# Performance work log

Hardware: AMD Instinct MI355X
Metric: run time of the kernel (lower is better)

The kernel has to match this reference:

```python
import jax, jax.numpy as jnp
import numpy as np

B, N, C = 4, 32768, 64
D_IN = B * C          # 256 == in_channels * batch_size
D_MODEL = 256
HEADS = 2
NUM_EDGES = 4096
N_INC = 131072
EPS = 1e-5
NEG = 0.2


def _leaky(v):
    return jnp.where(v >= 0, v, NEG * v)


def _bn(v, g, b, m, var):  # BatchNorm1d, eval mode (running stats)
    return g * (v - m) * jax.lax.rsqrt(var + EPS) + b


def setup_inputs() -> dict:
    key = jax.random.key(0)
    ks = jax.random.split(key, 16)

    def lin_init(k, fan_in, shape):
        lim = 1.0 / np.sqrt(fan_in)
        return jax.random.uniform(k, shape, jnp.float32, -lim, lim)

    x = jax.random.normal(ks[0], (B, N, C), jnp.float32)
    row_n = jax.random.randint(ks[1], (N_INC,), 0, N, jnp.int32)
    row_e = jax.random.randint(ks[2], (N_INC,), 0, NUM_EDGES, jnp.int32)
    row_e = row_e.at[0].set(NUM_EDGES - 1)  # guarantee max edge id -> num_edges
    hyperedge_all = jnp.stack([row_n, row_e])

    return {
        "x": x,
        "hyperedge_all": hyperedge_all,
        # linear1: d_in -> d_model
        "W1": lin_init(ks[3], D_IN, (D_MODEL, D_IN)),
        "b1": lin_init(ks[4], D_IN, (D_MODEL,)),
        "bn1_g": 1.0 + 0.1 * jax.random.normal(ks[5], (D_MODEL,), jnp.float32),
        "bn1_b": 0.1 * jax.random.normal(ks[6], (D_MODEL,), jnp.float32),
        "bn1_m": 0.01 * jax.random.normal(ks[7], (D_MODEL,), jnp.float32),
        "bn1_v": jnp.ones((D_MODEL,), jnp.float32),
        # HypergraphConv lin: d_model -> heads*d_model (no bias); att: [heads, 2*d_model]
        "attW": lin_init(ks[8], D_MODEL, (HEADS * D_MODEL, D_MODEL)),
        "att": 0.1 * jax.random.normal(ks[9], (HEADS, 2 * D_MODEL), jnp.float32),
        "cb": 0.01 * jax.random.normal(ks[10], (D_MODEL,), jnp.float32),
        "bn2_g": 1.0 + 0.1 * jax.random.normal(ks[11], (D_MODEL,), jnp.float32),
        "bn2_b": 0.1 * jax.random.normal(ks[12], (D_MODEL,), jnp.float32),
        "bn2_m": 0.01 * jax.random.normal(ks[13], (D_MODEL,), jnp.float32),
        "bn2_v": jnp.ones((D_MODEL,), jnp.float32),
        # linear2: d_model -> d_in
        "W2": lin_init(ks[14], D_MODEL, (D_IN, D_MODEL)),
        "b2": lin_init(ks[15], D_MODEL, (D_IN,)),
        "ln_g": jnp.ones((C,), jnp.float32),
        "ln_b": jnp.zeros((C,), jnp.float32),
    }


def reference(x, hyperedge_all, W1, b1, bn1_g, bn1_b, bn1_m, bn1_v,
              attW, att, cb, bn2_g, bn2_b, bn2_m, bn2_v, W2, b2, ln_g, ln_b):
    src = x
    h = x.reshape(N, B * C)                               # [N, D_IN] (raw row-major reshape, as torch)
    h = _leaky(h @ W1.T + b1)                             # [N, D_MODEL]
    h = _bn(h, bn1_g, bn1_b, bn1_m, bn1_v)

    idx_n = hyperedge_all[0]                              # [I] node index per incidence
    idx_e = hyperedge_all[1]                              # [I] hyperedge index per incidence

    # hyperedge_attr = A^T h where A is the (0/1, duplicate-summed) incidence matrix
    eattr = jax.ops.segment_sum(h[idx_n], idx_e, NUM_EDGES)            # [E, D_MODEL]

    # --- HypergraphConv with attention, concat=False ---
    xh = (h @ attW.T).reshape(N, HEADS, D_MODEL)                       # [N, H, D]
    ea = (eattr @ attW.T).reshape(NUM_EDGES, HEADS, D_MODEL)           # [E, H, D]
    att_n, att_e = att[:, :D_MODEL], att[:, D_MODEL:]                  # [H, D] each
    sn = jnp.einsum('nhd,hd->nh', xh, att_n)                           # node score
    se = jnp.einsum('ehd,hd->eh', ea, att_e)                           # edge score
    alpha = _leaky(sn[idx_n] + se[idx_e])                              # [I, H]
    # segment softmax over destination nodes (PyG softmax(alpha, hyperedge_index[0]))
    amax = jax.ops.segment_max(alpha, idx_n, N)
    amax = jnp.where(jnp.isfinite(amax), amax, 0.0)
    ex = jnp.exp(alpha - amax[idx_n])
    denom = jax.ops.segment_sum(ex, idx_n, N)
    alpha = ex / (denom[idx_n] + 1e-16)                                # [I, H]

    ones_i = jnp.ones((N_INC,), h.dtype)
    deg_n = jax.ops.segment_sum(ones_i, idx_n, N)                      # D (hyperedge_weight = 1)
    Dinv = jnp.where(deg_n > 0, 1.0 / deg_n, 0.0)
    deg_e = jax.ops.segment_sum(ones_i, idx_e, NUM_EDGES)              # B
    Binv = jnp.where(deg_e > 0, 1.0 / deg_e, 0.0)

    # node -> edge: edge_out[e] = sum_inc B[e] * alpha * xh[n]
    m1 = Binv[idx_e][:, None, None] * alpha[:, :, None] * xh[idx_n]    # [I, H, D]
    edge_out = jax.ops.segment_sum(m1, idx_e, NUM_EDGES)               # [E, H, D]
    # edge -> node: node_out[n] = sum_inc D[n] * alpha * edge_out[e]
    m2 = Dinv[idx_n][:, None, None] * alpha[:, :, None] * edge_out[idx_e]
    node_out = jax.ops.segment_sum(m2, idx_n, N)                       # [N, H, D]
    x2 = node_out.mean(axis=1) + cb                                    # concat=False -> head mean + bias

    h = _bn(h + x2, bn2_g, bn2_b, bn2_m, bn2_v)
    h = _leaky(h @ W2.T + b2)                                          # [N, D_IN]

    y = src + h.reshape(B, N, C)                                       # residual (raw reshape back)
    mu = y.mean(-1, keepdims=True)                                     # LayerNorm over C
    var = jnp.mean((y - mu) ** 2, -1, keepdims=True)
    return ln_g * (y - mu) * jax.lax.rsqrt(var + EPS) + ln_b
```

## Files before the change

kernel.cpp:

```cpp
#include <hip/hip_runtime.h>

#define NN 32768
#define EE 4096
#define NI 131072
#define NEGS 0.2f
#define EPSV 1e-5f

typedef __bf16 bf16;
typedef __bf16 bf16x8 __attribute__((ext_vector_type(8)));
typedef __bf16 bf16x4 __attribute__((ext_vector_type(4)));
typedef float f32x4 __attribute__((ext_vector_type(4)));

#define AS1 __attribute__((address_space(1)))
#define AS3 __attribute__((address_space(3)))

__device__ __forceinline__ void gld16(const void* g, void* l) {
    __builtin_amdgcn_global_load_lds((const AS1 unsigned*)g, (AS3 unsigned*)l, 16, 0, 0);
}

__device__ __forceinline__ void stage_hl(const bf16* WH, const bf16* WL, bf16* sW,
                                         int buf, int kk, int wave, int lane) {
#pragma unroll
    for (int i = 0; i < 4; ++i) {
        size_t goff = (size_t)(wave*64 + lane)*256 + (size_t)kk*32 + i*8;
        size_t lb = (size_t)buf*16384 + (size_t)(i*256 + wave*64)*8;
        gld16(WH + goff, sW + lb);
        gld16(WL + goff, sW + 8192 + lb);
    }
}

__device__ __forceinline__ void stage_w(const bf16* WB, bf16* sW,
                                        int buf, int kk, int wave, int lane) {
#pragma unroll
    for (int i = 0; i < 4; ++i) {
        gld16(WB + (size_t)(wave*64 + lane)*256 + (size_t)kk*32 + i*8,
              sW + (size_t)buf*8192 + (size_t)(i*256 + wave*64)*8);
    }
}

constexpr size_t OFF_FLAGS = 0;
constexpr size_t OFF_W1F   = 32;
constexpr size_t OFF_WAF   = OFF_W1F + 65536;
constexpr size_t OFF_W2F   = OFF_WAF + 131072;
constexpr size_t OFF_SN    = OFF_W2F + 65536;
constexpr size_t OFF_SE    = OFF_SN + (size_t)NN*2;
constexpr size_t OFF_ALPHA = OFF_SE + (size_t)EE*2;
constexpr size_t OFF_DENOM = OFF_ALPHA + (size_t)NI*2;
constexpr size_t OFF_DEGN  = OFF_DENOM + (size_t)NN*2;
constexpr size_t OFF_DEGE  = OFF_DEGN + (size_t)NN;
constexpr size_t OFF_EATTR = OFF_DEGE + (size_t)EE;
constexpr size_t OFF_EOUT  = OFF_EATTR + (size_t)EE*256;
constexpr size_t OFF_H     = OFF_EOUT + (size_t)EE*512;
constexpr size_t OFF_WBA2  = OFF_H + (size_t)NN*256;
constexpr size_t OFF_WN    = OFF_WBA2 + 65536;
constexpr size_t OFF_WE    = OFF_WN + 512;
constexpr size_t OFF_ECOFF = OFF_WE + 512;
constexpr size_t OFF_ECURS = OFF_ECOFF + 4100;
constexpr size_t OFF_ECLIST= OFF_ECURS + (size_t)EE;
constexpr size_t WS_TOTAL  = OFF_ECLIST + (size_t)NI;

__device__ __forceinline__ float leaky(float v) { return v < 0.f ? NEGS * v : v; }

__device__ __forceinline__ float rdv(const void* p, size_t i, int f) {
    return f ? (float)((const bf16*)p)[i] : ((const float*)p)[i];
}

__device__ __forceinline__ void rd_idx(const void* p, int i, int mode, int& n, int& e) {
    if (mode == 0)      { n = ((const int*)p)[i];            e = ((const int*)p)[NI + i]; }
    else if (mode == 2) { n = ((const int*)p)[2*i];          e = ((const int*)p)[2*i + 1]; }
    else if (mode == 1) { n = (int)((const long long*)p)[i]; e = (int)((const long long*)p)[NI + i]; }
    else if (mode == 3) { n = (int)((const float*)p)[i];     e = (int)((const float*)p)[NI + i]; }
    else                { n = 0; e = 0; }
    if ((unsigned)n >= NN) n = 0;
    if ((unsigned)e >= EE) e = 0;
}

__global__ void detect_kernel(const void* p0, const void* p2, const void* p3, const void* p4,
                              const void* p5, const void* p6, const void* p7, const void* p8,
                              const void* p9, const void* p10, const void* p11, const void* p12,
                              const void* p13, const void* p14, const void* p15, const void* p16,
                              const void* p17, const void* p18, int* F) {
    __shared__ int cnt;
    int b = blockIdx.x, t = threadIdx.x;
    const void* ps[19] = {p0, nullptr, p2, p3, p4, p5, p6, p7, p8, p9, p10,
                          p11, p12, p13, p14, p15, p16, p17, p18};
    const int scan[19] = {2048, 0, 2048, 256, 256, 256, 256, 0, 2048, 1024,
                          256, 256, 256, 256, 0, 256, 256, 0, 0};
    if (b == 1)  { if (t == 0) { F[1] = 1; F[26] = 0; F[27] = 0; F[28] = 0; F[29] = 0; } return; }
    if (b == 18) { if (t == 0) F[18] = 1; return; }
    if (b == 7 || b == 14 || b == 17) {
        if (t == 0) F[b] = (*(const unsigned*)ps[b] == 0x3F803F80u) ? 1 : 0;
        return;
    }
    if (t == 0) cnt = 0;
    __syncthreads();
    int n = scan[b];
    int local = 0;
    for (int i = t; i < n; i += 256) {
        unsigned short u = ((const unsigned short*)ps[b])[i];
        if (((u >> 7) & 0xFFu) >= 0xC0u) local = 1;
    }
    if (local) atomicAdd(&cnt, 1);
    __syncthreads();
    if (t == 0) F[b] = (cnt == 0) ? 1 : 0;
}

__global__ void k_setflags(int* F) {
    if (threadIdx.x == 0) {
        F[25] = (!F[26]) ? 0 : (!F[28]) ? 2 : (!F[27]) ? 1 : (!F[29]) ? 3 : 99;
        int a = 1;
        const int ids[18] = {0,2,3,4,5,6,7,8,9,10,11,12,13,14,15,16,17,18};
        for (int k = 0; k < 18; ++k) a &= F[ids[k]];
        F[20] = a;
    }
}

__global__ void k_idxcheck(const void* p, int* F) {
    int i = blockIdx.x * 256 + threadIdx.x;
    const int*       p32 = (const int*)p;
    const long long* p64 = (const long long*)p;
    const float*     pf  = (const float*)p;
    int n0 = p32[i], e0 = p32[NI + i];
    if ((unsigned)n0 >= NN || (unsigned)e0 >= EE) atomicOr(&F[26], 1);
    int n2 = p32[2*i], e2 = p32[2*i + 1];
    if ((unsigned)n2 >= NN || (unsigned)e2 >= EE) atomicOr(&F[28], 1);
    long long n1 = p64[i], e1 = p64[NI + i];
    if (n1 < 0 || n1 >= NN || e1 < 0 || e1 >= EE) atomicOr(&F[27], 1);
    float nf = pf[i], ef = pf[NI + i];
    if (!(nf >= 0.f && nf < (float)NN && nf == floorf(nf)) ||
        !(ef >= 0.f && ef < (float)EE && ef == floorf(ef))) atomicOr(&F[29], 1);
}

__global__ void marker_kernel(float* OUT, int code) {
    size_t i = (size_t)blockIdx.x * 256 + threadIdx.x;
    OUT[i] = (i == 1) ? (float)code : 0.f;
}

__global__ void convb_kernel(const void* src, bf16* dst, const int* F, int fidx) {
    size_t i = ((size_t)blockIdx.x * 256 + threadIdx.x) * 4;
    if (F[fidx]) {
        *(bf16x4*)(dst + i) = *(const bf16x4*)((const bf16*)src + i);
    } else {
        f32x4 v = *(const f32x4*)((const float*)src + i);
        bf16x4 o;
        o[0] = (bf16)v[0]; o[1] = (bf16)v[1]; o[2] = (bf16)v[2]; o[3] = (bf16)v[3];
        *(bf16x4*)(dst + i) = o;
    }
}

__global__ void k_w1conv(const void* W1, const int* F, bf16* WH, bf16* WL) {
    size_t i = (size_t)blockIdx.x * 256 + threadIdx.x;
    float w = rdv(W1, i, F[2]);
    bf16 h = (bf16)w;
    WH[i] = h;
    WL[i] = (bf16)(w - (float)h);
}

__global__ void k_prep2(const void* g2, const void* be2, const void* m2, const void* v2,
                        const void* cb, const int* F, float* ST) {
    int k = threadIdx.x;
    float s = rdv(g2, k, F[11]) * rsqrtf(rdv(v2, k, F[14]) + EPSV);
    float t = s * (rdv(cb, k, F[10]) - rdv(m2, k, F[13])) + rdv(be2, k, F[12]);
    ST[k] = s; ST[256 + k] = t;
}

__global__ void k_w2conv(const void* W2, const void* b2, const float* ST, const int* F,
                         bf16* WH, bf16* WL, float* B2P) {
    __shared__ float sacc[4];
    int c = blockIdx.x, k = threadIdx.x;
    float w  = rdv(W2, (size_t)c*256 + k, F[15]);
    float sw = ST[k] * w;
    bf16 h = (bf16)sw;
    WH[(size_t)c*256 + k] = h;
    WL[(size_t)c*256 + k] = (bf16)(sw - (float)h);
    float p = ST[256 + k] * w;
#pragma unroll
    for (int m = 32; m >= 1; m >>= 1) p += __shfl_xor(p, m, 64);
    int lane = k & 63, wv = k >> 6;
    if (lane == 0) sacc[wv] = p;
    __syncthreads();
    if (k == 0) B2P[c] = rdv(b2, c, F[16]) + sacc[0] + sacc[1] + sacc[2] + sacc[3];
}

__global__ void k_fold(const void* attW, const void* att, const int* F,
                       float* WN, float* WE) {
    int c = threadIdx.x;
    int h = blockIdx.y;
    int d0 = blockIdx.x * 16;
    int faw = F[8], fat = F[9];
    float swn = 0.f, swe = 0.f;
#pragma unroll 4
    for (int dd = 0; dd < 16; ++dd) {
        int d = d0 + dd;
        float w = rdv(attW, (size_t)(h*256 + d)*256 + c, faw);
        swn += w * rdv(att, h*512 + d, fat);
        swe += w * rdv(att, h*512 + 256 + d, fat);
    }
    atomicAdd(&WN[h*256 + c], swn);
    atomicAdd(&WE[h*256 + c], swe);
}

__global__ void k_deg(const void* __restrict__ idx, float* __restrict__ DEGN,
                      float* __restrict__ DEGE, const int* __restrict__ F) {
    int i = blockIdx.x * 256 + threadIdx.x;
    int n, e; rd_idx(idx, i, F[25], n, e);
    atomicAdd(&DEGN[n], 1.f);
    atomicAdd(&DEGE[e], 1.f);
}

__global__ void scan_a(const float* __restrict__ DEGN, const float* __restrict__ DEGE,
                       int* __restrict__ BS) {
    __shared__ int wsum[4];
    int b = blockIdx.x, t = threadIdx.x, lane = t & 63, wave = t >> 6;
    const float* DEG = (b < 32) ? DEGN + (size_t)b*1024 : DEGE + (size_t)(b-32)*1024;
    f32x4 v = *(const f32x4*)(DEG + (size_t)t*4);
    int s = (int)v[0] + (int)v[1] + (int)v[2] + (int)v[3];
#pragma unroll
    for (int m = 32; m >= 1; m >>= 1) s += __shfl_xor(s, m, 64);
    if (lane == 0) wsum[wave] = s;
    __syncthreads();
    if (t == 0) BS[b] = wsum[0] + wsum[1] + wsum[2] + wsum[3];
}

__global__ void scan_b2(int* BS) {
    if (threadIdx.x == 0) { int run = 0; for (int i = 0;  i < 32; ++i) { int s = BS[i]; BS[i] = run; run += s; } }
    if (threadIdx.x == 1) { int run = 0; for (int i = 32; i < 36; ++i) { int s = BS[i]; BS[i] = run; run += s; } }
}

__global__ void scan_c(float* __restrict__ DEGN, float* __restrict__ DEGE,
                       const int* __restrict__ BS,
                       int* __restrict__ NOFF, int* __restrict__ NCURS,
                       int* __restrict__ ECOFF, int* __restrict__ ECURS) {
    __shared__ int wsum[4];
    int b = blockIdx.x, t = threadIdx.x, lane = t & 63, wave = t >> 6;
    bool isN = (b < 32);
    int bb = isN ? b : b - 32;
    float* DEG = isN ? DEGN + (size_t)bb*1024 : DEGE + (size_t)bb*1024;
    int* OFF   = isN ? NOFF + bb*1024 : ECOFF + bb*1024;
    int* CURS  = isN ? NCURS + bb*1024 : ECURS + bb*1024;
    f32x4 v = *(const f32x4*)(DEG + (size_t)t*4);
    int c0 = (int)v[0], c1 = (int)v[1], c2 = (int)v[2], c3 = (int)v[3];
    int s = c0 + c1 + c2 + c3;
    int p = s;
#pragma unroll
    for (int off = 1; off < 64; off <<= 1) {
        int u = __shfl_up(p, off, 64);
        if (lane >= off) p += u;
    }
    if (lane == 63) wsum[wave] = p;
    __syncthreads();
    int wb = 0;
    for (int w = 0; w < wave; ++w) wb += wsum[w];
    int run = BS[b] + wb + p - s;
    int i0 = t*4;
    int cs[4] = {c0, c1, c2, c3};
#pragma unroll
    for (int j = 0; j < 4; ++j) {
        OFF[i0 + j] = run; CURS[i0 + j] = run; run += cs[j];
        DEG[i0 + j] = cs[j] > 0 ? 1.f / (float)cs[j] : 0.f;
    }
    if (t == 255 && (b == 31 || b == 35)) OFF[1024] = run;
}

__global__ __launch_bounds__(256) void k_h_mfma(const void* __restrict__ x,
                                                const bf16* __restrict__ WH,
                                                const bf16* __restrict__ WL,
                                                const void* b1, const void* g1, const void* be1,
                                                const void* m1, const void* v1,
                                                const float* __restrict__ WN,
                                                const float* __restrict__ WE,
                                                const int* __restrict__ F,
                                                float* __restrict__ H,
                                                float* __restrict__ SN,
                                                float* __restrict__ HE) {
    __shared__ float sB[256], sA[256], sM[256], sBE[256];
    __shared__ float sWN0[256], sWN1[256], sWE0[256], sWE1[256];
    __shared__ __align__(16) bf16 sW[32768];
    int tid = threadIdx.x;
    {
        sB[tid]  = rdv(b1, tid, F[3]);
        sA[tid]  = rdv(g1, tid, F[4]) * rsqrtf(rdv(v1, tid, F[7]) + EPSV);
        sM[tid]  = rdv(m1, tid, F[6]);
        sBE[tid] = rdv(be1, tid, F[5]);
        sWN0[tid] = WN[tid];
        sWN1[tid] = WN[256 + tid];
        sWE0[tid] = WE[tid];
        sWE1[tid] = WE[256 + tid];
    }
    int lane = tid & 63, wave = tid >> 6;
    int l15 = lane & 15, quad = lane >> 4;
    int row0 = (blockIdx.x * 4 + wave) * 16;
    int fx = F[0];
    const size_t abase = (size_t)(row0 + l15) * 256;
    f32x4 acc[16];
#pragma unroll
    for (int t = 0; t < 16; ++t) acc[t] = (f32x4){0.f, 0.f, 0.f, 0.f};
    stage_hl(WH, WL, sW, 0, 0, wave, lane);
    bf16x8 aNb; f32x4 aN0, aN1;
    if (fx) {
        aNb = *(const bf16x8*)((const bf16*)x + abase + quad*8);
    } else {
        aN0 = *(const f32x4*)((const float*)x + abase + quad*8);
        aN1 = *(const f32x4*)((const float*)x + abase + quad*8 + 4);
    }
    __syncthreads();
    int cur = 0;
    for (int kk = 0; kk < 8; ++kk) {
        if (kk < 7) stage_hl(WH, WL, sW, cur ^ 1, kk + 1, wave, lane);
        bf16x8 ah, al;
        if (fx) {
            ah = aNb;
            if (kk < 7) aNb = *(const bf16x8*)((const bf16*)x + abase + (kk+1)*32 + quad*8);
        } else {
            f32x4 a0 = aN0, a1 = aN1;
            if (kk < 7) {
                aN0 = *(const f32x4*)((const float*)x + abase + (kk+1)*32 + quad*8);
                aN1 = *(const f32x4*)((const float*)x + abase + (kk+1)*32 + quad*8 + 4);
            }
#pragma unroll
            for (int j = 0; j < 4; ++j) {
                bf16 h0 = (bf16)a0[j]; ah[j] = h0; al[j] = (bf16)(a0[j] - (float)h0);
                bf16 h1 = (bf16)a1[j]; ah[4+j] = h1; al[4+j] = (bf16)(a1[j] - (float)h1);
            }
        }
        const bf16* pH = sW + cur*16384 + quad*2048 + l15*8;
        const bf16* pL = pH + 8192;
#pragma unroll
        for (int t = 0; t < 16; ++t) {
            bf16x8 bh = *(const bf16x8*)(pH + t*128);
            bf16x8 bl = *(const bf16x8*)(pL + t*128);
            acc[t] = __builtin_amdgcn_mfma_f32_16x16x32_bf16(ah, bh, acc[t], 0, 0, 0);
            if (!fx) acc[t] = __builtin_amdgcn_mfma_f32_16x16x32_bf16(al, bh, acc[t], 0, 0, 0);
            acc[t] = __builtin_amdgcn_mfma_f32_16x16x32_bf16(ah, bl, acc[t], 0, 0, 0);
        }
        __syncthreads();
        cur ^= 1;
    }
    float p0[4] = {0.f,0.f,0.f,0.f}, p1[4] = {0.f,0.f,0.f,0.f};
    float q0[4] = {0.f,0.f,0.f,0.f}, q1[4] = {0.f,0.f,0.f,0.f};
#pragma unroll
    for (int t = 0; t < 16; ++t) {
        int cc = t*16 + l15;
        float A = sA[cc], Mv = sM[cc], BE = sBE[cc], Bv = sB[cc];
        float wn0 = sWN0[cc], wn1 = sWN1[cc], we0 = sWE0[cc], we1 = sWE1[cc];
#pragma unroll
        for (int r = 0; r < 4; ++r) {
            int rr = row0 + quad*4 + r;
            float v = leaky(acc[t][r] + Bv);
            float hv = A * (v - Mv) + BE;
            H[(size_t)rr*256 + cc] = hv;
            p0[r] += hv * wn0;
            p1[r] += hv * wn1;
            q0[r] += hv * we0;
            q1[r] += hv * we1;
        }
    }
#pragma unroll
    for (int r = 0; r < 4; ++r) {
#pragma unroll
        for (int m = 8; m >= 1; m >>= 1) {
            p0[r] += __shfl_xor(p0[r], m, 64);
            p1[r] += __shfl_xor(p1[r], m, 64);
            q0[r] += __shfl_xor(q0[r], m, 64);
            q1[r] += __shfl_xor(q1[r], m, 64);
        }
        if (l15 == 0) {
            int rr = row0 + quad*4 + r;
            SN[(size_t)rr*2]     = p0[r];
            SN[(size_t)rr*2 + 1] = p1[r];
            HE[(size_t)rr*2]     = q0[r];
            HE[(size_t)rr*2 + 1] = q1[r];
        }
    }
}

__global__ void k_se(const void* __restrict__ idx, const float* __restrict__ HE,
                     float* __restrict__ SE, const int* __restrict__ F) {
    int i = blockIdx.x * 256 + threadIdx.x;
    int n, e; rd_idx(idx, i, F[25], n, e);
    atomicAdd(&SE[(size_t)e*2],     HE[(size_t)n*2]);
    atomicAdd(&SE[(size_t)e*2 + 1], HE[(size_t)n*2 + 1]);
}

__global__ void k_alpha(const void* idx, const float* SN, const float* SE,
                        float* ALPHA, float* DENOM, int* NCURS, int* NLIST, const int* F) {
    int i = blockIdx.x * 256 + threadIdx.x;
    int n, e; rd_idx(idx, i, F[25], n, e);
    float e0 = expf(leaky(SN[(size_t)n*2]     + SE[(size_t)e*2]));
    float e1 = expf(leaky(SN[(size_t)n*2 + 1] + SE[(size_t)e*2 + 1]));
    ALPHA[(size_t)i*2] = e0; ALPHA[(size_t)i*2 + 1] = e1;
    atomicAdd(&DENOM[(size_t)n*2], e0);
    atomicAdd(&DENOM[(size_t)n*2 + 1], e1);
    int pos = atomicAdd(&NCURS[n], 1);
    NLIST[pos] = i;
}

__global__ void fill_e_k(const void* __restrict__ idx, int* __restrict__ CURS,
                         int* __restrict__ CLIST, const int* __restrict__ F) {
    int i = blockIdx.x * 256 + threadIdx.x;
    int n, e; rd_idx(idx, i, F[25], n, e);
    int pos = atomicAdd(&CURS[e], 1);
    CLIST[pos] = i;
}

__global__ __launch_bounds__(256) void m1g_csr_k(const int* __restrict__ COFF,
                                                 const int* __restrict__ CLIST,
                                                 const void* __restrict__ idx,
                                                 const float* __restrict__ ALPHA,
                                                 const float* __restrict__ DENOM,
                                                 const float* __restrict__ H,
                                                 float* __restrict__ G,
                                                 const int* __restrict__ F) {
    __shared__ int   s_n[64];
    __shared__ float s_c0[64];
    __shared__ float s_c1[64];
    int e = blockIdx.x, t = threadIdx.x;
    int beg = COFF[e], end = COFF[e + 1];
    float acc0 = 0.f, acc1 = 0.f;
    for (int base = beg; base < end; base += 64) {
        int cnt = min(64, end - base);
        if (t < cnt) {
            int i = CLIST[base + t];
            int n, ee; rd_idx(idx, i, F[25], n, ee);
            s_n[t]  = n;
            s_c0[t] = ALPHA[(size_t)i*2]     / (DENOM[(size_t)n*2]     + 1e-16f);
            s_c1[t] = ALPHA[(size_t)i*2 + 1] / (DENOM[(size_t)n*2 + 1] + 1e-16f);
        }
        __syncthreads();
        for (int k = 0; k < cnt; ++k) {
            float hv = H[(size_t)s_n[k]*256 + t];
            acc0 += s_c0[k] * hv;
            acc1 += s_c1[k] * hv;
        }
        __syncthreads();
    }
    G[(size_t)e*512 + t]       = acc0;
    G[(size_t)e*512 + 256 + t] = acc1;
}

__global__ __launch_bounds__(256) void gemm_eout_k(const float* __restrict__ G,
                                                   const bf16* __restrict__ WBA,
                                                   const float* __restrict__ BINV,
                                                   float* __restrict__ EOUT) {
    __shared__ __align__(16) bf16 sW[16384];
    int h = blockIdx.y;
    int tid = threadIdx.x, lane = tid & 63, wave = tid >> 6;
    int l15 = lane & 15, quad = lane >> 4;
    int row0 = blockIdx.x * 16;
    const float* Arow = G + (size_t)(row0 + l15) * 512 + h * 256;
    const bf16* WB = WBA + (size_t)h * 65536;
    f32x4 acc[4];
#pragma unroll
    for (int t = 0; t < 4; ++t) acc[t] = (f32x4){0.f, 0.f, 0.f, 0.f};
    stage_w(WB, sW, 0, 0, wave, lane);
    f32x4 aN0 = *(const f32x4*)(Arow + quad*8);
    f32x4 aN1 = *(const f32x4*)(Arow + quad*8 + 4);
    __syncthreads();
    int cur = 0;
    for (int kk = 0; kk < 8; ++kk) {
        if (kk < 7) stage_w(WB, sW, cur ^ 1, kk + 1, wave, lane);
        f32x4 a0 = aN0, a1 = aN1;
        if (kk < 7) {
            aN0 = *(const f32x4*)(Arow + (kk+1)*32 + quad*8);
            aN1 = *(const f32x4*)(Arow + (kk+1)*32 + quad*8 + 4);
        }
        bf16x8 a;
#pragma unroll
        for (int j = 0; j < 4; ++j) { a[j] = (bf16)a0[j]; a[4+j] = (bf16)a1[j]; }
        const bf16* pB = sW + cur*8192 + quad*2048 + l15*8;
#pragma unroll
        for (int tc = 0; tc < 4; ++tc) {
            int t = wave*4 + tc;
            bf16x8 b = *(const bf16x8*)(pB + t*128);
            acc[tc] = __builtin_amdgcn_mfma_f32_16x16x32_bf16(a, b, acc[tc], 0, 0, 0);
        }
        __syncthreads();
        cur ^= 1;
    }
#pragma unroll
    for (int tc = 0; tc < 4; ++tc) {
        int cc = (wave*4 + tc)*16 + l15;
#pragma unroll
        for (int r = 0; r < 4; ++r) {
            int e = row0 + quad*4 + r;
            EOUT[(size_t)e*512 + h*256 + cc] = acc[tc][r] * BINV[e];
        }
    }
}

__global__ __launch_bounds__(256) void k_m2g(const int* __restrict__ NOFF,
                                             const int* __restrict__ NLIST,
                                             const void* __restrict__ idx,
                                             const float* __restrict__ ALPHA,
                                             const float* __restrict__ DENOM,
                                             const float* __restrict__ DINV,
                                             const float* __restrict__ EOUT,
                                             float* __restrict__ H,
                                             const int* __restrict__ F) {
    __shared__ int   s_e[64];
    __shared__ float s_a0[64];
    __shared__ float s_a1[64];
    int n = blockIdx.x, t = threadIdx.x;
    int beg = NOFF[n], end = NOFF[n + 1];
    float dn0 = DENOM[(size_t)n*2]     + 1e-16f;
    float dn1 = DENOM[(size_t)n*2 + 1] + 1e-16f;
    float acc = 0.f;
    for (int base = beg; base < end; base += 64) {
        int cnt = min(64, end - base);
        if (t < cnt) {
            int i = NLIST[base + t];
            int nn, e; rd_idx(idx, i, F[25], nn, e);
            s_e[t]  = e;
            s_a0[t] = ALPHA[(size_t)i*2]     / dn0;
            s_a1[t] = ALPHA[(size_t)i*2 + 1] / dn1;
        }
        __syncthreads();
        for (int k = 0; k < cnt; ++k) {
            int e = s_e[k];
            acc += s_a0[k] * EOUT[(size_t)e*512 + t] + s_a1[k] * EOUT[(size_t)e*512 + 256 + t];
        }
        __syncthreads();
    }
    H[(size_t)n*256 + t] += 0.5f * DINV[n] * acc;
}

__global__ __launch_bounds__(256) void k_out_mfma(const float* __restrict__ H,
                                                  const bf16* __restrict__ WH,
                                                  const bf16* __restrict__ WL,
                                                  const float* __restrict__ B2P,
                                                  const void* __restrict__ x,
                                                  const void* lng, const void* lnb,
                                                  const int* __restrict__ F,
                                                  void* __restrict__ OUT) {
    __shared__ float sB2[256];
    __shared__ float sG[64], sBnd[64];
    __shared__ __align__(16) bf16 sW[32768];
    int tid = threadIdx.x;
    {
        sB2[tid] = B2P[tid];
        if (tid < 64) { sG[tid] = rdv(lng, tid, F[17]); sBnd[tid] = rdv(lnb, tid, F[18]); }
    }
    int lane = tid & 63, wave = tid >> 6;
    int l15 = lane & 15, quad = lane >> 4;
    int row0 = (blockIdx.x * 4 + wave) * 16;
    int fx = F[0], fo = F[20];
    const float* Arow = H + (size_t)(row0 + l15) * 256;
    f32x4 acc[16];
#pragma unroll
    for (int t = 0; t < 16; ++t) acc[t] = (f32x4){0.f, 0.f, 0.f, 0.f};
    stage_hl(WH, WL, sW, 0, 0, wave, lane);
    f32x4 aN0 = *(const f32x4*)(Arow + quad*8);
    f32x4 aN1 = *(const f32x4*)(Arow + quad*8 + 4);
    __syncthreads();
    int cur = 0;
    for (int kk = 0; kk < 8; ++kk) {
        if (kk < 7) stage_hl(WH, WL, sW, cur ^ 1, kk + 1, wave, lane);
        f32x4 a0 = aN0, a1 = aN1;
        if (kk < 7) {
            aN0 = *(const f32x4*)(Arow + (kk+1)*32 + quad*8);
            aN1 = *(const f32x4*)(Arow + (kk+1)*32 + quad*8 + 4);
        }
        bf16x8 ah, al;
#pragma unroll
        for (int j = 0; j < 4; ++j) {
            bf16 h0 = (bf16)a0[j]; ah[j] = h0; al[j] = (bf16)(a0[j] - (float)h0);
            bf16 h1 = (bf16)a1[j]; ah[4+j] = h1; al[4+j] = (bf16)(a1[j] - (float)h1);
        }
        const bf16* pH = sW + cur*16384 + quad*2048 + l15*8;
        const bf16* pL = pH + 8192;
#pragma unroll
        for (int t = 0; t < 16; ++t) {
            bf16x8 bh = *(const bf16x8*)(pH + t*128);
            bf16x8 bl = *(const bf16x8*)(pL + t*128);
            acc[t] = __builtin_amdgcn_mfma_f32_16x16x32_bf16(ah, bh, acc[t], 0, 0, 0);
            acc[t] = __builtin_amdgcn_mfma_f32_16x16x32_bf16(al, bh, acc[t], 0, 0, 0);
            acc[t] = __builtin_amdgcn_mfma_f32_16x16x32_bf16(ah, bl, acc[t], 0, 0, 0);
        }
        __syncthreads();
        cur ^= 1;
    }
#pragma unroll
    for (int t = 0; t < 16; ++t) {
        int cc = t*16 + l15;
        float Bv = sB2[cc];
#pragma unroll
        for (int r = 0; r < 4; ++r) {
            int rr = row0 + quad*4 + r;
            acc[t][r] = rdv(x, (size_t)rr*256 + cc, fx) + leaky(acc[t][r] + Bv);
        }
    }
#pragma unroll
    for (int r = 0; r < 4; ++r) {
        int rr = row0 + quad*4 + r;
#pragma unroll
        for (int g = 0; g < 4; ++g) {
            float s = acc[4*g][r] + acc[4*g+1][r] + acc[4*g+2][r] + acc[4*g+3][r];
            s += __shfl_xor(s, 1, 64); s += __shfl_xor(s, 2, 64);
            s += __shfl_xor(s, 4, 64); s += __shfl_xor(s, 8, 64);
            float mu = s * (1.f / 64.f);
            float q = 0.f;
#pragma unroll
            for (int j = 0; j < 4; ++j) { float d = acc[4*g+j][r] - mu; q += d * d; }
            q += __shfl_xor(q, 1, 64); q += __shfl_xor(q, 2, 64);
            q += __shfl_xor(q, 4, 64); q += __shfl_xor(q, 8, 64);
            float rsq = rsqrtf(q * (1.f / 64.f) + EPSV);
#pragma unroll
            for (int j = 0; j < 4; ++j) {
                int cc = (4*g + j)*16 + l15;
                int gi = cc & 63;
                float o = sG[gi] * (acc[4*g+j][r] - mu) * rsq + sBnd[gi];
                size_t idx = (size_t)rr*256 + cc;
                if (fo) ((bf16*)OUT)[idx] = (bf16)o;
                else    ((float*)OUT)[idx] = o;
            }
        }
    }
}

extern "C" void kernel_launch(void* const* d_in, const int* in_sizes, int n_in,
                              void* d_out, int out_size, void* d_ws, size_t ws_size,
                              hipStream_t stream) {
    float* ws = (float*)d_ws;
    int* F = (int*)(ws + OFF_FLAGS);

    if (ws_size < WS_TOTAL * sizeof(float)) {
        marker_kernel<<<NN, 256, 0, stream>>>((float*)d_out, 300);
        return;
    }
    if (n_in < 19) {
        marker_kernel<<<NN, 256, 0, stream>>>((float*)d_out, 355);
        return;
    }
    const int exp_sizes[19] = {8388608, 262144, 65536, 256, 256, 256, 256, 256, 131072,
                               1024, 256, 256, 256, 256, 256, 65536, 256, 64, 64};
    for (int i = 0; i < 19; ++i) {
        if (in_sizes[i] != exp_sizes[i]) {
            marker_kernel<<<NN, 256, 0, stream>>>((float*)d_out, 330 + i);
            return;
        }
    }

    float* ST    = ws + OFF_W1F;
    float* B2P   = ws + OFF_W1F + 512;
    int*   BS    = (int*)(ws + OFF_W1F + 768);
    int*   NCURS = (int*)(ws + OFF_W1F + 1024);
    int*   NOFF  = (int*)(ws + OFF_W2F);
    bf16*  W1H = (bf16*)(ws + OFF_WAF);
    bf16*  W1L = (bf16*)(ws + OFF_WAF + 32768);
    bf16*  W2H = (bf16*)(ws + OFF_WAF + 65536);
    bf16*  W2L = (bf16*)(ws + OFF_WAF + 98304);
    int*   ECOFF  = (int*)(ws + OFF_ECOFF);
    int*   ECURS  = (int*)(ws + OFF_ECURS);
    int*   CLIST  = (int*)(ws + OFF_ECLIST);
    float* HE     = ws + OFF_EATTR;
    int*   NLIST  = (int*)(ws + OFF_EATTR + 65536);

    hipMemsetAsync((char*)d_ws + OFF_SE * 4, 0, (OFF_EATTR - OFF_SE) * 4, stream);
    hipMemsetAsync((char*)d_ws + OFF_WN * 4, 0, 1024 * 4, stream);

    detect_kernel<<<19, 256, 0, stream>>>(d_in[0], d_in[2], d_in[3], d_in[4], d_in[5], d_in[6],
                                          d_in[7], d_in[8], d_in[9], d_in[10], d_in[11], d_in[12],
                                          d_in[13], d_in[14], d_in[15], d_in[16], d_in[17], d_in[18], F);
    k_idxcheck<<<NI/256, 256, 0, stream>>>(d_in[1], F);
    k_setflags<<<1, 64, 0, stream>>>(F);

    k_deg<<<NI/256, 256, 0, stream>>>(d_in[1], ws + OFF_DEGN, ws + OFF_DEGE, F);
    scan_a<<<36, 256, 0, stream>>>(ws + OFF_DEGN, ws + OFF_DEGE, BS);
    scan_b2<<<1, 64, 0, stream>>>(BS);
    scan_c<<<36, 256, 0, stream>>>(ws + OFF_DEGN, ws + OFF_DEGE, BS, NOFF, NCURS, ECOFF, ECURS);
    fill_e_k<<<NI/256, 256, 0, stream>>>(d_in[1], ECURS, CLIST, F);

    k_w1conv<<<256, 256, 0, stream>>>(d_in[2], F, W1H, W1L);
    convb_kernel<<<128, 256, 0, stream>>>(d_in[8], (bf16*)(ws + OFF_WBA2), F, 8);
    k_fold<<<dim3(16, 2), 256, 0, stream>>>(d_in[8], d_in[9], F, ws + OFF_WN, ws + OFF_WE);
    k_prep2<<<1, 256, 0, stream>>>(d_in[11], d_in[12], d_in[13], d_in[14], d_in[10], F, ST);
    k_w2conv<<<256, 256, 0, stream>>>(d_in[15], d_in[16], ST, F, W2H, W2L, B2P);

    k_h_mfma<<<NN/64, 256, 0, stream>>>(d_in[0], W1H, W1L, d_in[3], d_in[4], d_in[5],
                                        d_in[6], d_in[7], ws + OFF_WN, ws + OFF_WE, F,
                                        ws + OFF_H, ws + OFF_SN, HE);
    k_se<<<NI/256, 256, 0, stream>>>(d_in[1], HE, ws + OFF_SE, F);
    k_alpha<<<NI/256, 256, 0, stream>>>(d_in[1], ws + OFF_SN, ws + OFF_SE, ws + OFF_ALPHA,
                                        ws + OFF_DENOM, NCURS, NLIST, F);

    m1g_csr_k<<<EE, 256, 0, stream>>>(ECOFF, CLIST, d_in[1], ws + OFF_ALPHA, ws + OFF_DENOM,
                                      ws + OFF_H, ws + OFF_EOUT, F);

    gemm_eout_k<<<dim3(EE/16, 2), 256, 0, stream>>>(ws + OFF_EOUT, (const bf16*)(ws + OFF_WBA2),
                                                    ws + OFF_DEGE, ws + OFF_EOUT);

    k_m2g<<<NN, 256, 0, stream>>>(NOFF, NLIST, d_in[1], ws + OFF_ALPHA, ws + OFF_DENOM,
                                  ws + OFF_DEGN, ws + OFF_EOUT, ws + OFF_H, F);
    k_out_mfma<<<NN/64, 256, 0, stream>>>(ws + OFF_H, W2H, W2L, B2P, d_in[0],
                                          d_in[17], d_in[18], F, d_out);
}
```

Baseline: 471.8 us.

## Store edge intermediates in bf16 and fuse edge CSR fill into SE kernel

Writes the node-to-edge aggregate G and the edge outputs EOUT as bf16 instead of fp32. This halves the memory traffic of the per-node gather in k_m2g and of the GEMM input loads. The edge CSR list fill is merged into the SE atomic kernel, removing one launch and one pass over the incidence index. The cost is reduced precision of edge features and more atomic contention concentrated in one kernel.

Result: faster. 455.9 us (-3.4%).

```diff
diff --git a/kernel.cpp b/kernel.cpp
--- a/kernel.cpp
+++ b/kernel.cpp
@@ -374,12 +374,15 @@
     }
 }
 
-__global__ void k_se(const void* __restrict__ idx, const float* __restrict__ HE,
-                     float* __restrict__ SE, const int* __restrict__ F) {
+__global__ void k_sefill(const void* __restrict__ idx, const float* __restrict__ HE,
+                         float* __restrict__ SE, int* __restrict__ ECURS,
+                         int* __restrict__ CLIST, const int* __restrict__ F) {
     int i = blockIdx.x * 256 + threadIdx.x;
     int n, e; rd_idx(idx, i, F[25], n, e);
     atomicAdd(&SE[(size_t)e*2],     HE[(size_t)n*2]);
     atomicAdd(&SE[(size_t)e*2 + 1], HE[(size_t)n*2 + 1]);
+    int pos = atomicAdd(&ECURS[e], 1);
+    CLIST[pos] = i;
 }
 
 __global__ void k_alpha(const void* idx, const float* SN, const float* SE,
@@ -395,21 +398,13 @@
     NLIST[pos] = i;
 }
 
-__global__ void fill_e_k(const void* __restrict__ idx, int* __restrict__ CURS,
-                         int* __restrict__ CLIST, const int* __restrict__ F) {
-    int i = blockIdx.x * 256 + threadIdx.x;
-    int n, e; rd_idx(idx, i, F[25], n, e);
-    int pos = atomicAdd(&CURS[e], 1);
-    CLIST[pos] = i;
-}
-
 __global__ __launch_bounds__(256) void m1g_csr_k(const int* __restrict__ COFF,
                                                  const int* __restrict__ CLIST,
                                                  const void* __restrict__ idx,
                                                  const float* __restrict__ ALPHA,
                                                  const float* __restrict__ DENOM,
                                                  const float* __restrict__ H,
-                                                 float* __restrict__ G,
+                                                 bf16* __restrict__ G,
                                                  const int* __restrict__ F) {
     __shared__ int   s_n[64];
     __shared__ float s_c0[64];
@@ -434,39 +429,32 @@
         }
         __syncthreads();
     }
-    G[(size_t)e*512 + t]       = acc0;
-    G[(size_t)e*512 + 256 + t] = acc1;
-}
-
-__global__ __launch_bounds__(256) void gemm_eout_k(const float* __restrict__ G,
+    G[(size_t)e*512 + t]       = (bf16)acc0;
+    G[(size_t)e*512 + 256 + t] = (bf16)acc1;
+}
+
+__global__ __launch_bounds__(256) void gemm_eout_k(const bf16* __restrict__ G,
                                                    const bf16* __restrict__ WBA,
                                                    const float* __restrict__ BINV,
-                                                   float* __restrict__ EOUT) {
+                                                   bf16* __restrict__ EOUT) {
     __shared__ __align__(16) bf16 sW[16384];
     int h = blockIdx.y;
     int tid = threadIdx.x, lane = tid & 63, wave = tid >> 6;
     int l15 = lane & 15, quad = lane >> 4;
     int row0 = blockIdx.x * 16;
-    const float* Arow = G + (size_t)(row0 + l15) * 512 + h * 256;
+    const bf16* Arow = G + (size_t)(row0 + l15) * 512 + h * 256;
     const bf16* WB = WBA + (size_t)h * 65536;
     f32x4 acc[4];
 #pragma unroll
     for (int t = 0; t < 4; ++t) acc[t] = (f32x4){0.f, 0.f, 0.f, 0.f};
     stage_w(WB, sW, 0, 0, wave, lane);
-    f32x4 aN0 = *(const f32x4*)(Arow + quad*8);
-    f32x4 aN1 = *(const f32x4*)(Arow + quad*8 + 4);
+    bf16x8 aN = *(const bf16x8*)(Arow + quad*8);
     __syncthreads();
     int cur = 0;
     for (int kk = 0; kk < 8; ++kk) {
         if (kk < 7) stage_w(WB, sW, cur ^ 1, kk + 1, wave, lane);
-        f32x4 a0 = aN0, a1 = aN1;
-        if (kk < 7) {
-            aN0 = *(const f32x4*)(Arow + (kk+1)*32 + quad*8);
-            aN1 = *(const f32x4*)(Arow + (kk+1)*32 + quad*8 + 4);
-        }
-        bf16x8 a;
-#pragma unroll
-        for (int j = 0; j < 4; ++j) { a[j] = (bf16)a0[j]; a[4+j] = (bf16)a1[j]; }
+        bf16x8 a = aN;
+        if (kk < 7) aN = *(const bf16x8*)(Arow + (kk+1)*32 + quad*8);
         const bf16* pB = sW + cur*8192 + quad*2048 + l15*8;
 #pragma unroll
         for (int tc = 0; tc < 4; ++tc) {
@@ -483,7 +471,7 @@
 #pragma unroll
         for (int r = 0; r < 4; ++r) {
             int e = row0 + quad*4 + r;
-            EOUT[(size_t)e*512 + h*256 + cc] = acc[tc][r] * BINV[e];
+            EOUT[(size_t)e*512 + h*256 + cc] = (bf16)(acc[tc][r] * BINV[e]);
         }
     }
 }
@@ -494,7 +482,7 @@
                                              const float* __restrict__ ALPHA,
                                              const float* __restrict__ DENOM,
                                              const float* __restrict__ DINV,
-                                             const float* __restrict__ EOUT,
+                                             const bf16* __restrict__ EOUT,
                                              float* __restrict__ H,
                                              const int* __restrict__ F) {
     __shared__ int   s_e[64];
@@ -517,7 +505,8 @@
         __syncthreads();
         for (int k = 0; k < cnt; ++k) {
             int e = s_e[k];
-            acc += s_a0[k] * EOUT[(size_t)e*512 + t] + s_a1[k] * EOUT[(size_t)e*512 + 256 + t];
+            acc += s_a0[k] * (float)EOUT[(size_t)e*512 + t]
+                 + s_a1[k] * (float)EOUT[(size_t)e*512 + 256 + t];
         }
         __syncthreads();
     }
@@ -654,6 +643,8 @@
     int*   CLIST  = (int*)(ws + OFF_ECLIST);
     float* HE     = ws + OFF_EATTR;
     int*   NLIST  = (int*)(ws + OFF_EATTR + 65536);
+    bf16*  Gb     = (bf16*)(ws + OFF_EOUT);
+    bf16*  EOUTb  = (bf16*)(ws + OFF_EOUT + 1048576);
 
     hipMemsetAsync((char*)d_ws + OFF_SE * 4, 0, (OFF_EATTR - OFF_SE) * 4, stream);
     hipMemsetAsync((char*)d_ws + OFF_WN * 4, 0, 1024 * 4, stream);
@@ -668,7 +659,6 @@
     scan_a<<<36, 256, 0, stream>>>(ws + OFF_DEGN, ws + OFF_DEGE, BS);
     scan_b2<<<1, 64, 0, stream>>>(BS);
     scan_c<<<36, 256, 0, stream>>>(ws + OFF_DEGN, ws + OFF_DEGE, BS, NOFF, NCURS, ECOFF, ECURS);
-    fill_e_k<<<NI/256, 256, 0, stream>>>(d_in[1], ECURS, CLIST, F);
 
     k_w1conv<<<256, 256, 0, stream>>>(d_in[2], F, W1H, W1L);
     convb_kernel<<<128, 256, 0, stream>>>(d_in[8], (bf16*)(ws + OFF_WBA2), F, 8);
@@ -679,18 +669,18 @@
     k_h_mfma<<<NN/64, 256, 0, stream>>>(d_in[0], W1H, W1L, d_in[3], d_in[4], d_in[5],
                                         d_in[6], d_in[7], ws + OFF_WN, ws + OFF_WE, F,
                                         ws + OFF_H, ws + OFF_SN, HE);
-    k_se<<<NI/256, 256, 0, stream>>>(d_in[1], HE, ws + OFF_SE, F);
+    k_sefill<<<NI/256, 256, 0, stream>>>(d_in[1], HE, ws + OFF_SE, ECURS, CLIST, F);
     k_alpha<<<NI/256, 256, 0, stream>>>(d_in[1], ws + OFF_SN, ws + OFF_SE, ws + OFF_ALPHA,
                                         ws + OFF_DENOM, NCURS, NLIST, F);
 
     m1g_csr_k<<<EE, 256, 0, stream>>>(ECOFF, CLIST, d_in[1], ws + OFF_ALPHA, ws + OFF_DENOM,
-                                      ws + OFF_H, ws + OFF_EOUT, F);
-
-    gemm_eout_k<<<dim3(EE/16, 2), 256, 0, stream>>>(ws + OFF_EOUT, (const bf16*)(ws + OFF_WBA2),
-                                                    ws + OFF_DEGE, ws + OFF_EOUT);
+                                      ws + OFF_H, Gb, F);
+
+    gemm_eout_k<<<dim3(EE/16, 2), 256, 0, stream>>>(Gb, (const bf16*)(ws + OFF_WBA2),
+                                                    ws + OFF_DEGE, EOUTb);
 
     k_m2g<<<NN, 256, 0, stream>>>(NOFF, NLIST, d_in[1], ws + OFF_ALPHA, ws + OFF_DENOM,
-                                  ws + OFF_DEGN, ws + OFF_EOUT, ws + OFF_H, F);
+                                  ws + OFF_DEGN, EOUTb, ws + OFF_H, F);
     k_out_mfma<<<NN/64, 256, 0, stream>>>(ws + OFF_H, W2H, W2L, B2P, d_in[0],
                                           d_in[17], d_in[18], F, d_out);
 }
```
